# Performance work log

Hardware: AMD Instinct MI355X
Metric: run time of the kernel (lower is better)

The kernel has to match this reference:

```python
import jax, jax.numpy as jnp
import numpy as np
from math import sqrt

BS, SEQ, NV, DM, K = 16, 1024, 512, 256, 8
EPS = 0.05  # sinkhorn epsilon
TEMP = 0.07  # concrete-bernoulli temperature


def setup_inputs() -> dict:
    key = jax.random.key(0)
    k1, k2, k3 = jax.random.split(key, 3)
    x = jax.random.normal(k1, (BS, SEQ, NV), jnp.float32)
    # nn.Linear(seq_len, d_model): weight [d_model, seq_len], bias [d_model]
    W = jax.random.normal(k2, (DM, SEQ), jnp.float32) / sqrt(SEQ)
    b = jnp.zeros((DM,), jnp.float32)
    cluster_emb = jax.random.normal(k3, (K, DM), jnp.float32) / sqrt(DM)
    return {"x": x, "W": W, "b": b, "cluster_emb": cluster_emb}


def _l2norm(z):
    # F.normalize(x, dim=1, p=2) with eps=1e-12 clamp
    n = jnp.maximum(jnp.linalg.norm(z, axis=1, keepdims=True), 1e-12)
    return z / n


def _sinkhorn(q):
    Q = jnp.exp(q / EPS)
    return Q / jnp.sum(Q, axis=1, keepdims=True)


def _concrete_bern(p, key):
    u = jax.random.uniform(key, p.shape, p.dtype, 1e-10, 1.0 - 1e-10)
    noise = jnp.log(u) - jnp.log1p(-u)
    logit = jnp.log(p + 1e-10) - jnp.log(1.0 - p + 1e-10)
    return jax.nn.sigmoid((logit + noise) / TEMP)


def _forward(x, W, b, cluster_emb):
    bs, S, nv = x.shape
    d = W.shape[0]
    k = cluster_emb.shape[0]
    # permute -> [bs, nv, S], Linear(S -> d)
    x_emb = jnp.einsum('bsv,ds->bvd', x, W) + b  # [bs, nv, d]
    x_flat = x_emb.reshape(-1, d)  # [bs*nv, d]
    # cosine-similarity cluster logits
    prob = (_l2norm(x_flat) @ _l2norm(cluster_emb).T).reshape(bs, nv, k)
    prob_temp = _sinkhorn(prob.reshape(-1, k)).reshape(bs, nv, k)  # individual probs
    prob_avg = _sinkhorn(jnp.mean(prob, axis=0))  # [nv, k]
    mask = _concrete_bern(prob_avg, jax.random.key(42))  # [nv, k]
    # CrossAttention with n_heads=1 (dropout inactive in eval)
    scale = 1.0 / sqrt(d)
    scores = jnp.einsum('kd,bvd->bkv', cluster_emb, x_emb)  # [bs, k, nv]
    A = jax.nn.softmax(scale * scores, axis=-1) * mask.T[None]  # masked attn
    V = jnp.einsum('bkv,bvd->bkd', A, x_emb)  # [bs, k, d]
    cluster_emb_avg = jnp.mean(V, axis=0)  # [k, d] (stored attribute in torch)
    # cluster_base_encoding: straight-through bernoulli, broadcast over seq_len
    soft = prob_temp.transpose(2, 0, 1)[..., None]  # [k, bs, nv, 1]
    u = jax.random.uniform(jax.random.key(7), soft.shape, soft.dtype)
    bern = (u < jax.lax.stop_gradient(soft)).astype(soft.dtype)
    extend = jnp.broadcast_to(bern, (k, bs, nv, S))  # [k, bs, nv, S]
    hard = soft + jax.lax.stop_gradient(extend - soft)  # straight-through
    return hard


def reference(x, W, b, cluster_emb):
    return _forward(x, W, b, cluster_emb)
```

## Files before the change

kernel.cpp:

```cpp
#include <hip/hip_runtime.h>
#include <hip/hip_bf16.h>
#include <math.h>
#include <stdint.h>

#define BS 16
#define SEQ 1024
#define NV 512
#define DM 256
#define NK 8

__device__ double g_WC[NK * SEQ];
__device__ double g_Bk[NK];
__device__ double g_nn2p[4 * BS * NV];
__device__ double g_Dp[8 * BS * NV * NK];
__device__ unsigned char g_bits[BS * NV];

__device__ __forceinline__ void threefry2x32_key7(uint32_t x0, uint32_t x1,
                                                  uint32_t& o0, uint32_t& o1) {
    const uint32_t k0 = 0u, k1 = 7u;
    const uint32_t k2 = k0 ^ k1 ^ 0x1BD11BDAu;
    uint32_t v0 = x0 + k0, v1 = x1 + k1;
#define TF_ROUND(r) { v0 += v1; v1 = (v1 << (r)) | (v1 >> (32 - (r))); v1 ^= v0; }
    TF_ROUND(13) TF_ROUND(15) TF_ROUND(26) TF_ROUND(6)
    v0 += k1; v1 += k2 + 1u;
    TF_ROUND(17) TF_ROUND(29) TF_ROUND(16) TF_ROUND(24)
    v0 += k2; v1 += k0 + 2u;
    TF_ROUND(13) TF_ROUND(15) TF_ROUND(26) TF_ROUND(6)
    v0 += k0; v1 += k1 + 3u;
    TF_ROUND(17) TF_ROUND(29) TF_ROUND(16) TF_ROUND(24)
    v0 += k1; v1 += k2 + 4u;
    TF_ROUND(13) TF_ROUND(15) TF_ROUND(26) TF_ROUND(6)
    v0 += k2; v1 += k0 + 5u;
#undef TF_ROUND
    o0 = v0; o1 = v1;
}

__device__ __forceinline__ float bits_to_uniform(uint32_t b) {
    return __uint_as_float((b >> 9) | 0x3F800000u) - 1.0f;
}

__global__ __launch_bounds__(256) void prep_kernel(
        const float* __restrict__ W, const float* __restrict__ bias,
        const float* __restrict__ ce) {
    __shared__ double red[256];
    __shared__ double cen[256];
    const int t = threadIdx.x;
    const int k = blockIdx.x >> 2;
    const int schunk = blockIdx.x & 3;

    double c = (double)ce[k * DM + t];
    red[t] = c * c;
    __syncthreads();
    for (int off = 128; off > 0; off >>= 1) {
        if (t < off) red[t] += red[t + off];
        __syncthreads();
    }
    double nc = fmax(sqrt(red[0]), 1e-12);
    cen[t] = c / nc;
    __syncthreads();
    red[t] = (double)bias[t] * cen[t];
    __syncthreads();
    for (int off = 128; off > 0; off >>= 1) {
        if (t < off) red[t] += red[t + off];
        __syncthreads();
    }
    if (t == 0 && schunk == 0) g_Bk[k] = red[0];

    const int s = schunk * 256 + t;
    double acc = 0.0;
    for (int d = 0; d < DM; ++d)
        acc += cen[d] * (double)W[(size_t)d * SEQ + s];
    g_WC[(size_t)k * SEQ + s] = acc;
}

#define KC 32
#define XS_LD 132
#define WS_LD 68
#define ZS_LD 68

__global__ __launch_bounds__(256) void gemm_norm_kernel(
        const float* __restrict__ x, const float* __restrict__ W,
        const float* __restrict__ bias) {
    __shared__ __align__(16) char smem[43008];
    float* xs  = (float*)smem;
    float* wst = (float*)(smem + 16896);
    float* zS  = (float*)smem;
    double* pr = (double*)(smem + 34816);

    const int t = threadIdx.x;
    const int dblk = blockIdx.x;
    const int vblk = blockIdx.y;
    const int b    = blockIdx.z;
    const int v0 = vblk * 128, d0 = dblk * 64;
    const float* xb = x + (size_t)b * SEQ * NV;

    const int kh  = t >> 7;
    const int tid = t & 127;
    const int tv8 = (tid & 15) * 8;
    const int td8 = (tid >> 4) * 8;
    const int kb  = kh * 16;

    float acc[8][8];
#pragma unroll
    for (int j = 0; j < 8; ++j)
#pragma unroll
        for (int i = 0; i < 8; ++i) acc[j][i] = 0.0f;

    for (int s0 = 0; s0 < SEQ; s0 += KC) {
        __syncthreads();
#pragma unroll
        for (int j = 0; j < 4; ++j) {
            int lin = j * 256 + t;
            int sl = lin >> 5;
            int c4 = (lin & 31) << 2;
            float4 val = *(const float4*)&xb[(size_t)(s0 + sl) * NV + v0 + c4];
            *(float4*)&xs[sl * XS_LD + c4] = val;
        }
#pragma unroll
        for (int j = 0; j < 8; ++j) {
            int dl = (t >> 5) + 8 * j;
            int sl = t & 31;
            wst[sl * WS_LD + dl] = W[(size_t)(d0 + dl) * SEQ + s0 + sl];
        }
        __syncthreads();
#pragma unroll
        for (int kk = 0; kk < 16; ++kk) {
            const float* xr = &xs[(kb + kk) * XS_LD + tv8];
            const float* wr = &wst[(kb + kk) * WS_LD + td8];
            float4 xv0 = *(const float4*)(xr);
            float4 xv1 = *(const float4*)(xr + 4);
            float4 wv0 = *(const float4*)(wr);
            float4 wv1 = *(const float4*)(wr + 4);
            float xv[8] = {xv0.x, xv0.y, xv0.z, xv0.w, xv1.x, xv1.y, xv1.z, xv1.w};
            float wv[8] = {wv0.x, wv0.y, wv0.z, wv0.w, wv1.x, wv1.y, wv1.z, wv1.w};
#pragma unroll
            for (int j = 0; j < 8; ++j)
#pragma unroll
                for (int i = 0; i < 8; ++i) acc[j][i] += xv[j] * wv[i];
        }
    }

    __syncthreads();
    if (kh == 1) {
#pragma unroll
        for (int j = 0; j < 8; ++j) {
            *(float4*)&zS[(tv8 + j) * ZS_LD + td8]     =
                make_float4(acc[j][0], acc[j][1], acc[j][2], acc[j][3]);
            *(float4*)&zS[(tv8 + j) * ZS_LD + td8 + 4] =
                make_float4(acc[j][4], acc[j][5], acc[j][6], acc[j][7]);
        }
    }
    __syncthreads();
    if (kh == 0) {
        double bd[8];
#pragma unroll
        for (int i = 0; i < 8; ++i) bd[i] = (double)bias[d0 + td8 + i];
#pragma unroll
        for (int j = 0; j < 8; ++j) {
            double sq = 0.0;
#pragma unroll
            for (int i = 0; i < 8; ++i) {
                double z = (double)acc[j][i] +
                           (double)zS[(tv8 + j) * ZS_LD + td8 + i] + bd[i];
                sq += z * z;
            }
            pr[(tid >> 4) * 128 + tv8 + j] = sq;
        }
    }
    __syncthreads();
    if (t < 128) {
        double s = 0.0;
#pragma unroll
        for (int g = 0; g < 8; ++g) s += pr[g * 128 + t];
        g_nn2p[((size_t)dblk * BS + b) * NV + v0 + t] = s;
    }
}

__global__ __launch_bounds__(256) void dkern(const float* __restrict__ x) {
    __shared__ double wcd[NK][128];
    __shared__ double dw[4][64][NK];
    const int t = threadIdx.x;
    const int vblk = blockIdx.x;
    const int b    = blockIdx.y;
    const int sc   = blockIdx.z;
    const int v0 = vblk * 64;
    const int ss = sc * 128;

#pragma unroll
    for (int j = 0; j < 4; ++j) {
        int idx = j * 256 + t;
        ((double*)wcd)[idx] = g_WC[(size_t)(idx >> 7) * SEQ + ss + (idx & 127)];
    }
    __syncthreads();

    const int vl = t & 63, w = t >> 6;
    const float* xp = x + (size_t)b * SEQ * NV + v0 + vl;
    double D[NK];
#pragma unroll
    for (int k = 0; k < NK; ++k) D[k] = 0.0;
    const int sw = w * 32;
    for (int i = 0; i < 32; ++i) {
        int sl = sw + i;
        double xv = (double)xp[(size_t)(ss + sl) * NV];
#pragma unroll
        for (int k = 0; k < NK; ++k) D[k] += xv * wcd[k][sl];
    }
#pragma unroll
    for (int k = 0; k < NK; ++k) dw[w][vl][k] = D[k];
    __syncthreads();

    const int v = t & 63, k2 = (t >> 6) * 2;
#pragma unroll
    for (int j = 0; j < 2; ++j) {
        int k = k2 + j;
        double s = dw[0][v][k] + dw[1][v][k] + dw[2][v][k] + dw[3][v][k];
        g_Dp[(((size_t)sc * BS + b) * NV + v0 + v) * NK + k] = s;
    }
}

__global__ __launch_bounds__(256) void finalize_kernel() {
    const int bv = blockIdx.x * 256 + threadIdx.x;
    double nn2 = 0.0;
#pragma unroll
    for (int db = 0; db < 4; ++db) nn2 += g_nn2p[(size_t)db * (BS * NV) + bv];
    double n = fmax(sqrt(nn2), 1e-12);

    double D[NK];
#pragma unroll
    for (int k = 0; k < NK; ++k) D[k] = g_Bk[k];
#pragma unroll
    for (int sc = 0; sc < 8; ++sc) {
#pragma unroll
        for (int k = 0; k < NK; ++k)
            D[k] += g_Dp[((size_t)sc * (BS * NV) + bv) * NK + k];
    }

    double p[NK], sum = 0.0;
#pragma unroll
    for (int k = 0; k < NK; ++k) {
        p[k] = exp((D[k] / n) / 0.05);
        sum += p[k];
    }
    unsigned int byte = 0;
#pragma unroll
    for (int k = 0; k < NK; ++k) {
        uint32_t i = (uint32_t)(k * (BS * NV) + bv);
        uint32_t y0, y1;
        threefry2x32_key7(0u, i, y0, y1);
        float u = bits_to_uniform(y0 ^ y1);
        if ((double)u < p[k] / sum) byte |= 1u << k;
    }
    g_bits[bv] = (unsigned char)byte;
}

__global__ __launch_bounds__(256) void write_kernel(float* __restrict__ out) {
    const int t = threadIdx.x;
    const size_t r0 = (size_t)blockIdx.x * 8;
#pragma unroll
    for (int j = 0; j < 8; ++j) {
        size_t r = r0 + j;
        unsigned int bv = (unsigned int)(r & 8191u);
        unsigned int k  = (unsigned int)(r >> 13);
        float v = ((g_bits[bv] >> k) & 1u) ? 1.0f : 0.0f;
        float4 val = make_float4(v, v, v, v);
        ((float4*)(out + r * 1024))[t] = val;
    }
}

extern "C" void kernel_launch(void* const* d_in, const int* in_sizes, int n_in,
                              void* d_out, int out_size, void* d_ws, size_t ws_size,
                              hipStream_t stream) {
    const float* x    = (const float*)d_in[0];
    const float* W    = (const float*)d_in[1];
    const float* bias = (const float*)d_in[2];
    const float* ce   = (const float*)d_in[3];
    float* out = (float*)d_out;

    prep_kernel<<<dim3(32), dim3(256), 0, stream>>>(W, bias, ce);
    gemm_norm_kernel<<<dim3(4, 4, 16), dim3(256), 0, stream>>>(x, W, bias);
    dkern<<<dim3(8, 16, 8), dim3(256), 0, stream>>>(x);
    finalize_kernel<<<dim3(32), dim3(256), 0, stream>>>();
    write_kernel<<<dim3(8192), dim3(256), 0, stream>>>(out);
}
```

Before: 398.7 us.

## Split GEMM over sequence dimension and add combine kernel for norms

Splits the x·W GEMM's reduction over the sequence dimension into two halves, doubling the grid from 256 to 512 blocks. Partial fp32 products are written to a global buffer, and a new combine kernel adds the halves and the bias and computes the per-row squared norm. The aim is better occupancy across the GPU's compute units during the GEMM. In exchange it adds an extra kernel launch and about 16 MB of global write-then-read traffic, and the norm is now built from fp32 partial sums.

```diff
diff --git a/kernel.cpp b/kernel.cpp
--- a/kernel.cpp
+++ b/kernel.cpp
@@ -11,7 +11,8 @@
 
 __device__ double g_WC[NK * SEQ];
 __device__ double g_Bk[NK];
-__device__ double g_nn2p[4 * BS * NV];
+__device__ __align__(16) float g_zp[2 * 4 * BS * NV * 64];
+__device__ double g_nn2[BS * NV];
 __device__ double g_Dp[8 * BS * NV * NK];
 __device__ unsigned char g_bits[BS * NV];
 
@@ -78,17 +79,16 @@
 #define WS_LD 68
 #define ZS_LD 68
 
-__global__ __launch_bounds__(256) void gemm_norm_kernel(
-        const float* __restrict__ x, const float* __restrict__ W,
-        const float* __restrict__ bias) {
-    __shared__ __align__(16) char smem[43008];
+__global__ __launch_bounds__(256) void gemm_kernel(
+        const float* __restrict__ x, const float* __restrict__ W) {
+    __shared__ __align__(16) char smem[34816];
     float* xs  = (float*)smem;
     float* wst = (float*)(smem + 16896);
     float* zS  = (float*)smem;
-    double* pr = (double*)(smem + 34816);
-
-    const int t = threadIdx.x;
-    const int dblk = blockIdx.x;
+
+    const int t = threadIdx.x;
+    const int dblk = blockIdx.x & 3;
+    const int kblk = blockIdx.x >> 2;
     const int vblk = blockIdx.y;
     const int b    = blockIdx.z;
     const int v0 = vblk * 128, d0 = dblk * 64;
@@ -106,7 +106,8 @@
 #pragma unroll
         for (int i = 0; i < 8; ++i) acc[j][i] = 0.0f;
 
-    for (int s0 = 0; s0 < SEQ; s0 += KC) {
+    const int sbeg = kblk * 512;
+    for (int s0 = sbeg; s0 < sbeg + 512; s0 += KC) {
         __syncthreads();
 #pragma unroll
         for (int j = 0; j < 4; ++j) {
@@ -152,27 +153,51 @@
     }
     __syncthreads();
     if (kh == 0) {
-        double bd[8];
-#pragma unroll
-        for (int i = 0; i < 8; ++i) bd[i] = (double)bias[d0 + td8 + i];
 #pragma unroll
         for (int j = 0; j < 8; ++j) {
-            double sq = 0.0;
-#pragma unroll
-            for (int i = 0; i < 8; ++i) {
-                double z = (double)acc[j][i] +
-                           (double)zS[(tv8 + j) * ZS_LD + td8 + i] + bd[i];
-                sq += z * z;
-            }
-            pr[(tid >> 4) * 128 + tv8 + j] = sq;
-        }
-    }
-    __syncthreads();
-    if (t < 128) {
+            float zrow[8];
+#pragma unroll
+            for (int i = 0; i < 8; ++i)
+                zrow[i] = acc[j][i] + zS[(tv8 + j) * ZS_LD + td8 + i];
+            size_t rowbase =
+                ((((size_t)kblk * 4 + dblk) * BS + b) * NV + v0 + tv8 + j) * 64 + td8;
+            *(float4*)&g_zp[rowbase]     = make_float4(zrow[0], zrow[1], zrow[2], zrow[3]);
+            *(float4*)&g_zp[rowbase + 4] = make_float4(zrow[4], zrow[5], zrow[6], zrow[7]);
+        }
+    }
+}
+
+__global__ __launch_bounds__(256) void combine_kernel(
+        const float* __restrict__ bias) {
+    __shared__ double red[16][17];
+    const int t = threadIdx.x;
+    const int vg = blockIdx.x;
+    const int b  = blockIdx.y;
+    const int vl = t >> 4, dg = t & 15;
+    const int v = vg * 16 + vl;
+    const int dblk = dg >> 2, dl0 = (dg & 3) * 16;
+
+    const size_t base0 = ((((size_t)0 * 4 + dblk) * BS + b) * NV + v) * 64 + dl0;
+    const size_t base1 = ((((size_t)1 * 4 + dblk) * BS + b) * NV + v) * 64 + dl0;
+    double sq = 0.0;
+#pragma unroll
+    for (int m = 0; m < 16; m += 4) {
+        float4 a  = *(const float4*)&g_zp[base0 + m];
+        float4 c  = *(const float4*)&g_zp[base1 + m];
+        float4 bb = *(const float4*)&bias[dg * 16 + m];
+        double z0 = (double)a.x + (double)c.x + (double)bb.x;
+        double z1 = (double)a.y + (double)c.y + (double)bb.y;
+        double z2 = (double)a.z + (double)c.z + (double)bb.z;
+        double z3 = (double)a.w + (double)c.w + (double)bb.w;
+        sq += z0 * z0 + z1 * z1 + z2 * z2 + z3 * z3;
+    }
+    red[vl][dg] = sq;
+    __syncthreads();
+    if (dg == 0) {
         double s = 0.0;
 #pragma unroll
-        for (int g = 0; g < 8; ++g) s += pr[g * 128 + t];
-        g_nn2p[((size_t)dblk * BS + b) * NV + v0 + t] = s;
+        for (int i = 0; i < 16; ++i) s += red[vl][i];
+        g_nn2[b * NV + v] = s;
     }
 }
 
@@ -220,10 +245,7 @@
 
 __global__ __launch_bounds__(256) void finalize_kernel() {
     const int bv = blockIdx.x * 256 + threadIdx.x;
-    double nn2 = 0.0;
-#pragma unroll
-    for (int db = 0; db < 4; ++db) nn2 += g_nn2p[(size_t)db * (BS * NV) + bv];
-    double n = fmax(sqrt(nn2), 1e-12);
+    double n = fmax(sqrt(g_nn2[bv]), 1e-12);
 
     double D[NK];
 #pragma unroll
@@ -277,7 +299,8 @@
     float* out = (float*)d_out;
 
     prep_kernel<<<dim3(32), dim3(256), 0, stream>>>(W, bias, ce);
-    gemm_norm_kernel<<<dim3(4, 4, 16), dim3(256), 0, stream>>>(x, W, bias);
+    gemm_kernel<<<dim3(8, 4, 16), dim3(256), 0, stream>>>(x, W);
+    combine_kernel<<<dim3(32, 16), dim3(256), 0, stream>>>(bias);
     dkern<<<dim3(8, 16, 8), dim3(256), 0, stream>>>(x);
     finalize_kernel<<<dim3(32), dim3(256), 0, stream>>>();
     write_kernel<<<dim3(8192), dim3(256), 0, stream>>>(out);
```

Measured after the change: 395.5 us. No clear change (-0.8%).
